# Kernel optimization log

Hardware: AMD Instinct MI355X
Metric: run time of the kernel (lower is better)

## Reference

```python
import jax, jax.numpy as jnp
import numpy as np

B, S, D, H = 2, 4096, 512, 8
HD = D // H

def setup_inputs() -> dict:
    key = jax.random.key(0)
    ks = jax.random.split(key, 11)
    s = 1.0 / np.sqrt(D)
    return {
        "x": jax.random.normal(ks[0], (B, S, D), jnp.float32),
        "y": jax.random.normal(ks[1], (B, S, D), jnp.float32),
        "z": jax.random.normal(ks[2], (B, S, D), jnp.float32),
        "Wq": jax.random.normal(ks[3], (D, D), jnp.float32) * s,
        "bq": jnp.zeros((D,), jnp.float32),
        "Wk": jax.random.normal(ks[4], (D, D), jnp.float32) * s,
        "bk": jnp.zeros((D,), jnp.float32),
        "Wv": jax.random.normal(ks[5], (D, D), jnp.float32) * s,
        "bv": jnp.zeros((D,), jnp.float32),
        "Wp": jax.random.normal(ks[6], (D, D), jnp.float32) * s,
        "bp": jnp.zeros((D,), jnp.float32),
    }

def reference(x, y, z, Wq, bq, Wk, bk, Wv, bv, Wp, bp):
    # q/k/v projections, split heads: [B,S,D] -> [B,H,S,HD]
    def heads(t):
        return t.reshape(B, -1, H, HD).transpose(0, 2, 1, 3)
    q = heads(x @ Wq + bq)
    k = heads(y @ Wk + bk)
    v = heads(z @ Wv + bv)
    att = jnp.einsum('bhqd,bhkd->bhqk', q, k) / np.sqrt(HD).astype(np.float32)
    att = jax.nn.softmax(att, axis=-1)  # dropout is identity in eval mode
    out = jnp.einsum('bhqk,bhkd->bhqd', att, v)
    out = out.transpose(0, 2, 1, 3).reshape(B, -1, D)
    return out @ Wp + bp
```

## Files before the change

### kernel.cpp

```cpp
#include <hip/hip_runtime.h>
#include <math.h>

#define B_ 2
#define S_ 4096
#define D_ 512
#define H_ 8
#define HD_ 64
#define NROW_ (B_ * S_)
#define NELEM_ ((size_t)NROW_ * D_)
#define WELEM_ ((size_t)D_ * D_)

#define LOG2E_ 1.44269504f
#define SCLAMP_ 15.869645f

typedef _Float16 half8 __attribute__((ext_vector_type(8)));
typedef _Float16 half4v __attribute__((ext_vector_type(4)));
typedef __fp16 fp16x2 __attribute__((ext_vector_type(2)));
typedef float floatx4 __attribute__((ext_vector_type(4)));
typedef float floatx16 __attribute__((ext_vector_type(16)));
typedef int intx2 __attribute__((ext_vector_type(2)));
typedef unsigned uintx4 __attribute__((ext_vector_type(4)));

__device__ __forceinline__ half8 cvt_half8(float4 a, float4 b) {
  fp16x2 l0 = __builtin_amdgcn_cvt_pkrtz(a.x, a.y);
  fp16x2 l1 = __builtin_amdgcn_cvt_pkrtz(a.z, a.w);
  fp16x2 l2 = __builtin_amdgcn_cvt_pkrtz(b.x, b.y);
  fp16x2 l3 = __builtin_amdgcn_cvt_pkrtz(b.z, b.w);
  half8 h;
  h[0] = l0[0]; h[1] = l0[1]; h[2] = l1[0]; h[3] = l1[1];
  h[4] = l2[0]; h[5] = l2[1]; h[6] = l3[0]; h[7] = l3[1];
  return h;
}

__device__ __forceinline__ void permswap32(unsigned& a, unsigned& b) {
#if __has_builtin(__builtin_amdgcn_permlane32_swap)
  intx2 r = __builtin_amdgcn_permlane32_swap((int)a, (int)b, false, false);
  a = (unsigned)r[0];
  b = (unsigned)r[1];
#else
  asm volatile("v_permlane32_swap_b32 %0, %1" : "+v"(a), "+v"(b));
#endif
}

__device__ __forceinline__ float exp2_hw(float x) {
  float r;
  asm("v_exp_f32 %0, %1" : "=v"(r) : "v"(x));
  return r;
}

struct WPtrs { const float *W0, *W1, *W2, *W3; };

__global__ void wT4_kernel(WPtrs p, _Float16* __restrict__ WTbase) {
  __shared__ float tl[32][33];
  const int z = blockIdx.z;
  const float* W = z == 0 ? p.W0 : z == 1 ? p.W1 : z == 2 ? p.W2 : p.W3;
  const float scale = z == 0 ? 0.125f * LOG2E_ : 1.0f;
  _Float16* Wt = WTbase + (size_t)z * WELEM_;
  const int t = threadIdx.x;
  const int k0 = blockIdx.y * 32, n0 = blockIdx.x * 32;
  const int r = t >> 3, c0 = (t & 7) * 4;
  const float4 v = *(const float4*)&W[(size_t)(k0 + r) * D_ + n0 + c0];
  tl[r][c0 + 0] = v.x; tl[r][c0 + 1] = v.y;
  tl[r][c0 + 2] = v.z; tl[r][c0 + 3] = v.w;
  __syncthreads();
  half4v hv;
#pragma unroll
  for (int j = 0; j < 4; ++j) hv[j] = (_Float16)(tl[c0 + j][r] * scale);
  *(half4v*)&Wt[(size_t)(n0 + r) * D_ + k0 + c0] = hv;
}

__global__ __launch_bounds__(256) void xcvt_kernel(
    const float* __restrict__ X0, const float* __restrict__ X1,
    _Float16* __restrict__ Xh) {
  const size_t e0 = (size_t)blockIdx.x * 8192;
  const float* src = e0 < NELEM_ ? X0 + e0 : X1 + (e0 - NELEM_);
  _Float16* dst = Xh + e0;
  const float4* s4 = (const float4*)src;
  const int t = threadIdx.x;
#pragma unroll
  for (int j = 0; j < 4; ++j) {
    const int i8 = j * 256 + t;
    const float4 a = s4[2 * i8];
    const float4 b = s4[2 * i8 + 1];
    *(half8*)&dst[(size_t)i8 * 8] = cvt_half8(a, b);
  }
}

template <bool AF16, int OUTMODE, int BM>
__device__ __forceinline__ void gemm_body(
    const void* __restrict__ Av, const _Float16* __restrict__ Bt,
    const float* __restrict__ bias, void* __restrict__ Cout, float bscale,
    _Float16* pool, int bx, int by, int tid) {
  constexpr int MT = BM / 32;
  _Float16 (*As)[72] = (_Float16 (*)[72])pool;
  _Float16 (*Bs)[72] = (_Float16 (*)[72])(pool + BM * 72);

  const int w = tid >> 6, lane = tid & 63;
  const int m = lane & 15, quad = lane >> 4;
  const int row0 = by * BM, col0 = bx * 128;
  const int wr = (w >> 1) * (BM / 2), wc = (w & 1) * 64;
  const int srow = tid >> 3, soff = (tid & 7) * 8;

  const _Float16* A16 = (const _Float16*)Av;
  const float* A32 = (const float*)Av;

  floatx4 acc[MT][4];
#pragma unroll
  for (int i = 0; i < MT; ++i)
#pragma unroll
    for (int j = 0; j < 4; ++j) acc[i][j] = floatx4{0.f, 0.f, 0.f, 0.f};

  half8 pa16[MT];
  float4 pa32[MT][2];
  half8 pb[4];
#pragma unroll
  for (int i = 0; i < MT; ++i) {
    const size_t ar = (size_t)(row0 + srow + 32 * i) * D_ + soff;
    if (AF16) pa16[i] = *(const half8*)&A16[ar];
    else { pa32[i][0] = *(const float4*)&A32[ar];
           pa32[i][1] = *(const float4*)&A32[ar + 4]; }
  }
#pragma unroll
  for (int i = 0; i < 4; ++i)
    pb[i] = *(const half8*)&Bt[(size_t)(col0 + srow + 32 * i) * D_ + soff];

  for (int kt = 0; kt < D_ / 64; ++kt) {
    if (kt) __syncthreads();
#pragma unroll
    for (int i = 0; i < MT; ++i)
      *(half8*)&As[srow + 32 * i][soff] =
          AF16 ? pa16[i] : cvt_half8(pa32[i][0], pa32[i][1]);
#pragma unroll
    for (int i = 0; i < 4; ++i) *(half8*)&Bs[srow + 32 * i][soff] = pb[i];
    __syncthreads();
    if (kt < D_ / 64 - 1) {
      const int kc = (kt + 1) * 64 + soff;
#pragma unroll
      for (int i = 0; i < MT; ++i) {
        const size_t ar = (size_t)(row0 + srow + 32 * i) * D_ + kc;
        if (AF16) pa16[i] = *(const half8*)&A16[ar];
        else { pa32[i][0] = *(const float4*)&A32[ar];
               pa32[i][1] = *(const float4*)&A32[ar + 4]; }
      }
#pragma unroll
      for (int i = 0; i < 4; ++i)
        pb[i] = *(const half8*)&Bt[(size_t)(col0 + srow + 32 * i) * D_ + kc];
    }
#pragma unroll
    for (int h = 0; h < 2; ++h) {
      half8 af[MT], bf[4];
#pragma unroll
      for (int mt = 0; mt < MT; ++mt)
        af[mt] = *(const half8*)&As[wr + mt * 16 + m][h * 32 + quad * 8];
#pragma unroll
      for (int nt = 0; nt < 4; ++nt)
        bf[nt] = *(const half8*)&Bs[wc + nt * 16 + m][h * 32 + quad * 8];
#pragma unroll
      for (int mt = 0; mt < MT; ++mt)
#pragma unroll
        for (int nt = 0; nt < 4; ++nt)
          acc[mt][nt] = __builtin_amdgcn_mfma_f32_16x16x32_f16(
              af[mt], bf[nt], acc[mt][nt], 0, 0, 0);
    }
  }

  float bv[4];
#pragma unroll
  for (int nt = 0; nt < 4; ++nt)
    bv[nt] = bias[col0 + wc + nt * 16 + m] * bscale;

  if constexpr (OUTMODE == 2) {
    __syncthreads();
    _Float16 (*Ct)[132] = (_Float16 (*)[132])pool;
#pragma unroll
    for (int mt = 0; mt < MT; ++mt)
#pragma unroll
      for (int nt = 0; nt < 4; ++nt)
#pragma unroll
        for (int r = 0; r < 4; ++r)
          Ct[wr + mt * 16 + quad * 4 + r][wc + nt * 16 + m] =
              (_Float16)(acc[mt][nt][r] + bv[nt]);
    __syncthreads();
    const int c = tid & 127, sc = tid >> 7;
    const int head = (col0 + c) >> 6, dd = (col0 + c) & 63;
    const int b = row0 >> 12;
    const int sbase = (row0 & (S_ - 1)) + sc * 64;
    _Float16* dst = (_Float16*)Cout +
        ((size_t)(b * H_ + head) * HD_ + dd) * S_ + sbase;
#pragma unroll
    for (int j = 0; j < 8; ++j) {
      half8 o;
#pragma unroll
      for (int e = 0; e < 8; ++e) o[e] = Ct[sc * 64 + j * 8 + e][c];
      *(half8*)&dst[j * 8] = o;
    }
  } else {
#pragma unroll
    for (int mt = 0; mt < MT; ++mt)
#pragma unroll
      for (int nt = 0; nt < 4; ++nt)
#pragma unroll
        for (int r = 0; r < 4; ++r) {
          const int row = row0 + wr + mt * 16 + quad * 4 + r;
          const int col = col0 + wc + nt * 16 + m;
          const float vout = acc[mt][nt][r] + bv[nt];
          if (OUTMODE == 1)
            ((_Float16*)Cout)[(size_t)row * D_ + col] = (_Float16)vout;
          else
            ((float*)Cout)[(size_t)row * D_ + col] = vout;
        }
  }
}

struct QkvPtrs { const float *A2, *b0, *b1, *b2; };

__global__ __launch_bounds__(256, 3) void qkv_gemm_kernel(
    QkvPtrs p, const _Float16* __restrict__ WT, _Float16* __restrict__ Cb,
    _Float16* __restrict__ VhT, const _Float16* __restrict__ Xh) {
  __shared__ alignas(16) _Float16 pool[(128 + 128) * 72];
  const int z = blockIdx.z;
  if (z == 2)
    gemm_body<false, 2, 128>(p.A2, WT + 2 * WELEM_, p.b2, VhT, 1.0f, pool,
                             blockIdx.x, blockIdx.y, threadIdx.x);
  else
    gemm_body<true, 1, 128>(Xh + (size_t)z * NELEM_, WT + (size_t)z * WELEM_,
                            z == 0 ? p.b0 : p.b1, Cb + (size_t)z * NELEM_,
                            z == 0 ? 0.125f * LOG2E_ : 1.0f, pool,
                            blockIdx.x, blockIdx.y, threadIdx.x);
}

__global__ __launch_bounds__(256, 3) void out_gemm_kernel(
    const _Float16* __restrict__ Oh, const _Float16* __restrict__ WpT,
    const float* __restrict__ bp, float* __restrict__ out) {
  __shared__ alignas(16) _Float16 pool[(64 + 128) * 72];
  gemm_body<true, 0, 64>(Oh, WpT, bp, out, 1.0f, pool, blockIdx.x,
                         blockIdx.y, threadIdx.x);
}

__global__ __launch_bounds__(512, 4) void attn_mfma_kernel(
    const _Float16* __restrict__ Qg, const _Float16* __restrict__ Kg,
    const _Float16* __restrict__ VT, _Float16* __restrict__ Og) {
  __shared__ alignas(16) unsigned char smem[73728];
  _Float16 (*Ks)[2][64][72] =
      reinterpret_cast<_Float16 (*)[2][64][72]>(smem);
  _Float16 (*Vt)[2][64][72] =
      reinterpret_cast<_Float16 (*)[2][64][72]>(smem + 36864);
  float (*comb)[64][36] = (float (*)[64][36])smem;

  const int t = threadIdx.x;
  const int w = t >> 6;
  const int g = w >> 2;
  const int wq = w & 3;
  const int lane = t & 63;
  const int li = lane & 31;
  const int hl = lane >> 5;
  const int q0 = blockIdx.x * 128 + wq * 32;
  const int koff = g * (S_ / 2);
  const size_t base =
      (size_t)blockIdx.z * ((size_t)S_ * D_) + (size_t)blockIdx.y * HD_;
  const size_t vbase = (size_t)(blockIdx.z * H_ + blockIdx.y) * HD_ * S_;

  half8 qb[4];
#pragma unroll
  for (int ks = 0; ks < 4; ++ks)
    qb[ks] = *(const half8*)
        &Qg[base + (size_t)(q0 + li) * D_ + ks * 16 + hl * 8];

  floatx16 oacc[2];
#pragma unroll
  for (int i = 0; i < 16; ++i) { oacc[0][i] = 0.f; oacc[1][i] = 0.f; }
  float lpart = 0.f;

  const int tg = t & 255;
  const int srow = tg >> 3, soff = (tg & 7) * 8;

#pragma unroll
  for (int i = 0; i < 2; ++i) {
    *(half8*)&Ks[g][0][srow + 32 * i][soff] = *(const half8*)
        &Kg[base + (size_t)(koff + srow + 32 * i) * D_ + soff];
    *(half8*)&Vt[g][0][srow + 32 * i][soff] = *(const half8*)
        &VT[vbase + (size_t)(srow + 32 * i) * S_ + koff + soff];
  }
  half8 pk[2], pv[2];
#pragma unroll
  for (int i = 0; i < 2; ++i) {
    pk[i] = *(const half8*)
        &Kg[base + (size_t)(koff + 64 + srow + 32 * i) * D_ + soff];
    pv[i] = *(const half8*)
        &VT[vbase + (size_t)(srow + 32 * i) * S_ + koff + 64 + soff];
  }
  __syncthreads();

  constexpr int NT2 = S_ / 128;
  for (int kt = 0; kt < NT2; ++kt) {
    const int cur = kt & 1;
    if (kt + 1 < NT2) {
#pragma unroll
      for (int i = 0; i < 2; ++i) {
        *(half8*)&Ks[g][cur ^ 1][srow + 32 * i][soff] = pk[i];
        *(half8*)&Vt[g][cur ^ 1][srow + 32 * i][soff] = pv[i];
      }
      if (kt + 2 < NT2) {
        const int k2 = koff + (kt + 2) * 64;
#pragma unroll
        for (int i = 0; i < 2; ++i) {
          pk[i] = *(const half8*)
              &Kg[base + (size_t)(k2 + srow + 32 * i) * D_ + soff];
          pv[i] = *(const half8*)
              &VT[vbase + (size_t)(srow + 32 * i) * S_ + k2 + soff];
        }
      }
    }

    floatx16 sacc[2];
#pragma unroll
    for (int i = 0; i < 16; ++i) { sacc[0][i] = 0.f; sacc[1][i] = 0.f; }
    __builtin_amdgcn_s_setprio(1);
#pragma unroll
    for (int ks = 0; ks < 4; ++ks) {
      const half8 ka0 = *(const half8*)&Ks[g][cur][li][ks * 16 + hl * 8];
      const half8 ka1 = *(const half8*)&Ks[g][cur][32 + li][ks * 16 + hl * 8];
      sacc[0] = __builtin_amdgcn_mfma_f32_32x32x16_f16(ka0, qb[ks],
                                                       sacc[0], 0, 0, 0);
      sacc[1] = __builtin_amdgcn_mfma_f32_32x32x16_f16(ka1, qb[ks],
                                                       sacc[1], 0, 0, 0);
    }
    __builtin_amdgcn_s_setprio(0);

#pragma unroll
    for (int kt2 = 0; kt2 < 2; ++kt2) {
      unsigned dq[4][2];
#pragma unroll
      for (int rq = 0; rq < 4; ++rq)
#pragma unroll
        for (int pp = 0; pp < 2; ++pp) {
          const float e0 =
              exp2_hw(fminf(sacc[kt2][4 * rq + 2 * pp], SCLAMP_));
          const float e1 =
              exp2_hw(fminf(sacc[kt2][4 * rq + 2 * pp + 1], SCLAMP_));
          lpart += e0 + e1;
          const fp16x2 h2 = __builtin_amdgcn_cvt_pkrtz(e0, e1);
          dq[rq][pp] = __builtin_bit_cast(unsigned, h2);
        }
      half8 pf[2];
#pragma unroll
      for (int t2 = 0; t2 < 2; ++t2) {
        unsigned a0 = dq[2 * t2][0], b0 = dq[2 * t2 + 1][0];
        unsigned a1 = dq[2 * t2][1], b1 = dq[2 * t2 + 1][1];
        permswap32(a0, b0);
        permswap32(a1, b1);
        uintx4 u; u[0] = a0; u[1] = a1; u[2] = b0; u[3] = b1;
        pf[t2] = __builtin_bit_cast(half8, u);
      }
      __builtin_amdgcn_s_setprio(1);
#pragma unroll
      for (int t2 = 0; t2 < 2; ++t2) {
        const int ks = 2 * kt2 + t2;
        const half8 va0 = *(const half8*)&Vt[g][cur][li][ks * 16 + hl * 8];
        const half8 va1 =
            *(const half8*)&Vt[g][cur][32 + li][ks * 16 + hl * 8];
        oacc[0] = __builtin_amdgcn_mfma_f32_32x32x16_f16(va0, pf[t2],
                                                         oacc[0], 0, 0, 0);
        oacc[1] = __builtin_amdgcn_mfma_f32_32x32x16_f16(va1, pf[t2],
                                                         oacc[1], 0, 0, 0);
      }
      __builtin_amdgcn_s_setprio(0);
    }

    __syncthreads();
  }

  const float wsum = lpart + __shfl_xor(lpart, 32);

  if (g == 1) {
#pragma unroll
    for (int n = 0; n < 2; ++n)
#pragma unroll
      for (int c = 0; c < 4; ++c) {
        float4 f;
        f.x = oacc[n][4 * c + 0]; f.y = oacc[n][4 * c + 1];
        f.z = oacc[n][4 * c + 2]; f.w = oacc[n][4 * c + 3];
        *(float4*)&comb[wq][lane][n * 16 + 4 * c] = f;
      }
    comb[wq][lane][32] = wsum;
  }
  __syncthreads();
  if (g == 0) {
    const float linv = 1.0f / (wsum + comb[wq][lane][32]);
#pragma unroll
    for (int n = 0; n < 2; ++n)
#pragma unroll
      for (int rq = 0; rq < 4; ++rq) {
        const float4 cf = *(const float4*)&comb[wq][lane][n * 16 + 4 * rq];
        half4v o4;
        o4[0] = (_Float16)((oacc[n][4 * rq + 0] + cf.x) * linv);
        o4[1] = (_Float16)((oacc[n][4 * rq + 1] + cf.y) * linv);
        o4[2] = (_Float16)((oacc[n][4 * rq + 2] + cf.z) * linv);
        o4[3] = (_Float16)((oacc[n][4 * rq + 3] + cf.w) * linv);
        *(half4v*)&Og[base + (size_t)(q0 + li) * D_ +
                      n * 32 + 8 * rq + 4 * hl] = o4;
      }
  }
}

extern "C" void kernel_launch(void* const* d_in, const int* in_sizes, int n_in,
                              void* d_out, int out_size, void* d_ws,
                              size_t ws_size, hipStream_t stream) {
  const float* x  = (const float*)d_in[0];
  const float* y  = (const float*)d_in[1];
  const float* z  = (const float*)d_in[2];
  const float* Wq = (const float*)d_in[3];
  const float* bq = (const float*)d_in[4];
  const float* Wk = (const float*)d_in[5];
  const float* bk = (const float*)d_in[6];
  const float* Wv = (const float*)d_in[7];
  const float* bv = (const float*)d_in[8];
  const float* Wp = (const float*)d_in[9];
  const float* bp = (const float*)d_in[10];

  _Float16* hws = (_Float16*)d_ws;
  _Float16* WT  = hws;
  _Float16* Xh  = WT + 4 * WELEM_;
  _Float16* Qh  = Xh + 2 * NELEM_;
  _Float16* Kh  = Qh + NELEM_;
  _Float16* VhT = Kh + NELEM_;
  _Float16* Oh  = Xh;

  WPtrs wp{Wq, Wk, Wv, Wp};
  wT4_kernel<<<dim3(16, 16, 4), 256, 0, stream>>>(wp, WT);

  xcvt_kernel<<<dim3(1024), 256, 0, stream>>>(x, y, Xh);

  QkvPtrs qp{z, bq, bk, bv};
  qkv_gemm_kernel<<<dim3(4, 64, 3), 256, 0, stream>>>(qp, WT, Qh, VhT, Xh);

  attn_mfma_kernel<<<dim3(S_ / 128, H_, B_), 512, 0, stream>>>(Qh, Kh, VhT, Oh);

  out_gemm_kernel<<<dim3(4, 128), 256, 0, stream>>>(Oh, WT + 3 * WELEM_, bp,
                                                    (float*)d_out);
}
```

Baseline: 241.1 us.

## Use direct global-to-LDS loads with XOR swizzle for fp16 GEMM tiles

Adds a path in the shared GEMM body that moves A and B tiles straight from global memory into LDS with global_load_lds, skipping the register staging and the separate LDS store. The LDS tiles become unpadded 64-wide rows, and an XOR swizzle on the 16-byte slot avoids bank conflicts when fragments are read. The Q/K projection and the output projection use this path; the fp32 V path keeps the old scheme. The old register prefetch of the next k-tile is dropped, so loads for a tile are no longer overlapped with the previous tile's MFMA work, which could expose load latency.

```diff
diff --git a/kernel.cpp b/kernel.cpp
--- a/kernel.cpp
+++ b/kernel.cpp
@@ -46,6 +46,12 @@
   float r;
   asm("v_exp_f32 %0, %1" : "=v"(r) : "v"(x));
   return r;
+}
+
+typedef const unsigned __attribute__((address_space(1))) gu32_t;
+typedef unsigned __attribute__((address_space(3))) lu32_t;
+__device__ __forceinline__ void gload16(const void* g, void* l) {
+  __builtin_amdgcn_global_load_lds((gu32_t*)g, (lu32_t*)l, 16, 0, 0);
 }
 
 struct WPtrs { const float *W0, *W1, *W2, *W3; };
@@ -86,20 +92,16 @@
   }
 }
 
-template <bool AF16, int OUTMODE, int BM>
+template <bool AF16, int OUTMODE, int BM, bool GL>
 __device__ __forceinline__ void gemm_body(
     const void* __restrict__ Av, const _Float16* __restrict__ Bt,
     const float* __restrict__ bias, void* __restrict__ Cout, float bscale,
     _Float16* pool, int bx, int by, int tid) {
   constexpr int MT = BM / 32;
-  _Float16 (*As)[72] = (_Float16 (*)[72])pool;
-  _Float16 (*Bs)[72] = (_Float16 (*)[72])(pool + BM * 72);
-
   const int w = tid >> 6, lane = tid & 63;
   const int m = lane & 15, quad = lane >> 4;
   const int row0 = by * BM, col0 = bx * 128;
   const int wr = (w >> 1) * (BM / 2), wc = (w & 1) * 64;
-  const int srow = tid >> 3, soff = (tid & 7) * 8;
 
   const _Float16* A16 = (const _Float16*)Av;
   const float* A32 = (const float*)Av;
@@ -110,57 +112,105 @@
 #pragma unroll
     for (int j = 0; j < 4; ++j) acc[i][j] = floatx4{0.f, 0.f, 0.f, 0.f};
 
-  half8 pa16[MT];
-  float4 pa32[MT][2];
-  half8 pb[4];
-#pragma unroll
-  for (int i = 0; i < MT; ++i) {
-    const size_t ar = (size_t)(row0 + srow + 32 * i) * D_ + soff;
-    if (AF16) pa16[i] = *(const half8*)&A16[ar];
-    else { pa32[i][0] = *(const float4*)&A32[ar];
-           pa32[i][1] = *(const float4*)&A32[ar + 4]; }
-  }
-#pragma unroll
-  for (int i = 0; i < 4; ++i)
-    pb[i] = *(const half8*)&Bt[(size_t)(col0 + srow + 32 * i) * D_ + soff];
-
-  for (int kt = 0; kt < D_ / 64; ++kt) {
-    if (kt) __syncthreads();
-#pragma unroll
-    for (int i = 0; i < MT; ++i)
-      *(half8*)&As[srow + 32 * i][soff] =
-          AF16 ? pa16[i] : cvt_half8(pa32[i][0], pa32[i][1]);
-#pragma unroll
-    for (int i = 0; i < 4; ++i) *(half8*)&Bs[srow + 32 * i][soff] = pb[i];
-    __syncthreads();
-    if (kt < D_ / 64 - 1) {
-      const int kc = (kt + 1) * 64 + soff;
-#pragma unroll
-      for (int i = 0; i < MT; ++i) {
-        const size_t ar = (size_t)(row0 + srow + 32 * i) * D_ + kc;
-        if (AF16) pa16[i] = *(const half8*)&A16[ar];
-        else { pa32[i][0] = *(const float4*)&A32[ar];
-               pa32[i][1] = *(const float4*)&A32[ar + 4]; }
-      }
-#pragma unroll
-      for (int i = 0; i < 4; ++i)
-        pb[i] = *(const half8*)&Bt[(size_t)(col0 + srow + 32 * i) * D_ + kc];
-    }
-#pragma unroll
-    for (int h = 0; h < 2; ++h) {
-      half8 af[MT], bf[4];
-#pragma unroll
-      for (int mt = 0; mt < MT; ++mt)
-        af[mt] = *(const half8*)&As[wr + mt * 16 + m][h * 32 + quad * 8];
-#pragma unroll
-      for (int nt = 0; nt < 4; ++nt)
-        bf[nt] = *(const half8*)&Bs[wc + nt * 16 + m][h * 32 + quad * 8];
-#pragma unroll
-      for (int mt = 0; mt < MT; ++mt)
+  if constexpr (GL) {
+    _Float16 (*Asl)[64] = (_Float16 (*)[64])pool;
+    _Float16 (*Bsl)[64] = (_Float16 (*)[64])(pool + BM * 64);
+    for (int kt = 0; kt < D_ / 64; ++kt) {
+      if (kt) __syncthreads();
+      const int kc = kt * 64;
+#pragma unroll
+      for (int i = 0; i < BM / 32; ++i) {
+        const int rb = (i * 4 + w) * 8;
+        const int row = rb + (lane >> 3);
+        const int slot = (lane & 7) ^ (row & 7);
+        gload16(&A16[(size_t)(row0 + row) * D_ + kc + slot * 8], &Asl[rb][0]);
+      }
+#pragma unroll
+      for (int i = 0; i < 4; ++i) {
+        const int rb = (i * 4 + w) * 8;
+        const int row = rb + (lane >> 3);
+        const int slot = (lane & 7) ^ (row & 7);
+        gload16(&Bt[(size_t)(col0 + row) * D_ + kc + slot * 8], &Bsl[rb][0]);
+      }
+      __syncthreads();
+#pragma unroll
+      for (int h = 0; h < 2; ++h) {
+        half8 af[MT], bf[4];
+#pragma unroll
+        for (int mt = 0; mt < MT; ++mt) {
+          const int r = wr + mt * 16 + m;
+          af[mt] = *(const half8*)&Asl[r][(((4 * h + quad) ^ (r & 7)) * 8)];
+        }
+#pragma unroll
+        for (int nt = 0; nt < 4; ++nt) {
+          const int r = wc + nt * 16 + m;
+          bf[nt] = *(const half8*)&Bsl[r][(((4 * h + quad) ^ (r & 7)) * 8)];
+        }
+#pragma unroll
+        for (int mt = 0; mt < MT; ++mt)
+#pragma unroll
+          for (int nt = 0; nt < 4; ++nt)
+            acc[mt][nt] = __builtin_amdgcn_mfma_f32_16x16x32_f16(
+                af[mt], bf[nt], acc[mt][nt], 0, 0, 0);
+      }
+    }
+  } else {
+    _Float16 (*As)[72] = (_Float16 (*)[72])pool;
+    _Float16 (*Bs)[72] = (_Float16 (*)[72])(pool + BM * 72);
+    const int srow = tid >> 3, soff = (tid & 7) * 8;
+
+    half8 pa16[MT];
+    float4 pa32[MT][2];
+    half8 pb[4];
+#pragma unroll
+    for (int i = 0; i < MT; ++i) {
+      const size_t ar = (size_t)(row0 + srow + 32 * i) * D_ + soff;
+      if (AF16) pa16[i] = *(const half8*)&A16[ar];
+      else { pa32[i][0] = *(const float4*)&A32[ar];
+             pa32[i][1] = *(const float4*)&A32[ar + 4]; }
+    }
+#pragma unroll
+    for (int i = 0; i < 4; ++i)
+      pb[i] = *(const half8*)&Bt[(size_t)(col0 + srow + 32 * i) * D_ + soff];
+
+    for (int kt = 0; kt < D_ / 64; ++kt) {
+      if (kt) __syncthreads();
+#pragma unroll
+      for (int i = 0; i < MT; ++i)
+        *(half8*)&As[srow + 32 * i][soff] =
+            AF16 ? pa16[i] : cvt_half8(pa32[i][0], pa32[i][1]);
+#pragma unroll
+      for (int i = 0; i < 4; ++i) *(half8*)&Bs[srow + 32 * i][soff] = pb[i];
+      __syncthreads();
+      if (kt < D_ / 64 - 1) {
+        const int kc = (kt + 1) * 64 + soff;
+#pragma unroll
+        for (int i = 0; i < MT; ++i) {
+          const size_t ar = (size_t)(row0 + srow + 32 * i) * D_ + kc;
+          if (AF16) pa16[i] = *(const half8*)&A16[ar];
+          else { pa32[i][0] = *(const float4*)&A32[ar];
+                 pa32[i][1] = *(const float4*)&A32[ar + 4]; }
+        }
+#pragma unroll
+        for (int i = 0; i < 4; ++i)
+          pb[i] = *(const half8*)&Bt[(size_t)(col0 + srow + 32 * i) * D_ + kc];
+      }
+#pragma unroll
+      for (int h = 0; h < 2; ++h) {
+        half8 af[MT], bf[4];
+#pragma unroll
+        for (int mt = 0; mt < MT; ++mt)
+          af[mt] = *(const half8*)&As[wr + mt * 16 + m][h * 32 + quad * 8];
 #pragma unroll
         for (int nt = 0; nt < 4; ++nt)
-          acc[mt][nt] = __builtin_amdgcn_mfma_f32_16x16x32_f16(
-              af[mt], bf[nt], acc[mt][nt], 0, 0, 0);
+          bf[nt] = *(const half8*)&Bs[wc + nt * 16 + m][h * 32 + quad * 8];
+#pragma unroll
+        for (int mt = 0; mt < MT; ++mt)
+#pragma unroll
+          for (int nt = 0; nt < 4; ++nt)
+            acc[mt][nt] = __builtin_amdgcn_mfma_f32_16x16x32_f16(
+                af[mt], bf[nt], acc[mt][nt], 0, 0, 0);
+      }
     }
   }
 
@@ -220,21 +270,22 @@
   __shared__ alignas(16) _Float16 pool[(128 + 128) * 72];
   const int z = blockIdx.z;
   if (z == 2)
-    gemm_body<false, 2, 128>(p.A2, WT + 2 * WELEM_, p.b2, VhT, 1.0f, pool,
-                             blockIdx.x, blockIdx.y, threadIdx.x);
+    gemm_body<false, 2, 128, false>(p.A2, WT + 2 * WELEM_, p.b2, VhT, 1.0f,
+                                    pool, blockIdx.x, blockIdx.y, threadIdx.x);
   else
-    gemm_body<true, 1, 128>(Xh + (size_t)z * NELEM_, WT + (size_t)z * WELEM_,
-                            z == 0 ? p.b0 : p.b1, Cb + (size_t)z * NELEM_,
-                            z == 0 ? 0.125f * LOG2E_ : 1.0f, pool,
-                            blockIdx.x, blockIdx.y, threadIdx.x);
+    gemm_body<true, 1, 128, true>(Xh + (size_t)z * NELEM_,
+                                  WT + (size_t)z * WELEM_,
+                                  z == 0 ? p.b0 : p.b1, Cb + (size_t)z * NELEM_,
+                                  z == 0 ? 0.125f * LOG2E_ : 1.0f, pool,
+                                  blockIdx.x, blockIdx.y, threadIdx.x);
 }
 
 __global__ __launch_bounds__(256, 3) void out_gemm_kernel(
     const _Float16* __restrict__ Oh, const _Float16* __restrict__ WpT,
     const float* __restrict__ bp, float* __restrict__ out) {
   __shared__ alignas(16) _Float16 pool[(64 + 128) * 72];
-  gemm_body<true, 0, 64>(Oh, WpT, bp, out, 1.0f, pool, blockIdx.x,
-                         blockIdx.y, threadIdx.x);
+  gemm_body<true, 0, 64, true>(Oh, WpT, bp, out, 1.0f, pool, blockIdx.x,
+                               blockIdx.y, threadIdx.x);
 }
 
 __global__ __launch_bounds__(512, 4) void attn_mfma_kernel(
```

Result: no change. 241.5 us (+0.2%).
